# Optimization experiments

Hardware: AMD Instinct MI355X
Metric: run time of the kernel (lower is better)

## Reference

```python
import jax, jax.numpy as jnp
import numpy as np

N = 4096   # patients
D = 256    # encoding dim per modality
EPS = 1e-8 # torch CosineSimilarity eps


def setup_inputs() -> dict:
    key = jax.random.key(0)
    ks = jax.random.split(key, 7)
    return {
        "log_hazard": jax.random.normal(ks[0], (N,), dtype=jnp.float32),
        "time": jax.random.randint(ks[1], (N,), 0, 3650, dtype=jnp.int32),
        "event": jax.random.randint(ks[2], (N,), 0, 2, dtype=jnp.int32),
        "eb0": jax.random.normal(ks[3], (N, D), dtype=jnp.float32),
        "eb1": jax.random.normal(ks[4], (N, D), dtype=jnp.float32),
        "eb2": jax.random.normal(ks[5], (N, D), dtype=jnp.float32),
        "eb3": jax.random.normal(ks[6], (N, D), dtype=jnp.float32),
        "M_margin": 1,
    }


def _cox_npll(h, t, e):
    # risk_matrix = (outer(t,t) >= t^2).T  ->  risk[i,j] = (t_j * t_i >= t_i^2)
    tt = t[:, None] * t[None, :]                      # [N,N] = t_i * t_j
    risk = (tt >= (t * t)[:, None]).astype(h.dtype)   # row i: patients j with t_j >= t_i
    log_denom = jnp.log(risk @ jnp.exp(h))            # [N]
    ef = e.astype(h.dtype)
    return -jnp.sum(ef * (h - log_denom)) / jnp.sum(ef)


def _similarity_loss(blocks, margin):
    # Vectorized form of the O(N^2 * n_mod) pairwise loop.
    matched = jnp.zeros((N, N), dtype=blocks[0].dtype)  # sum_mod cos(x_i, x_j) over valid mods
    own = jnp.zeros((N, N), dtype=blocks[0].dtype)      # sum_mod cos(x_i, x_i) over valid mods
    for x in blocks:
        nrm = jnp.linalg.norm(x, axis=1)                # [N]
        den = jnp.maximum(nrm, EPS)
        xn = x / den[:, None]
        S = xn @ xn.T                                   # cos(x_i, x_j) with torch eps semantics
        diag = (nrm * nrm) / (den * den)                # cos(x_i, x_i)
        miss = jnp.all(x == x[:, :1], axis=1)           # modality missing (constant row)
        valid = (~(miss[:, None] | miss[None, :])).astype(x.dtype)
        matched = matched + valid * S
        own = own + valid * diag[:, None]
    offdiag = 1.0 - jnp.eye(N, dtype=matched.dtype)
    per_pair = jax.nn.relu(margin - matched + own)
    return jnp.sum(offdiag * per_pair)


def reference(log_hazard, time, event, eb0, eb1, eb2, eb3, M_margin):
    margin = jnp.float32(M_margin)
    cox = _cox_npll(log_hazard, time, event)
    sim = _similarity_loss([eb0, eb1, eb2, eb3], margin)
    return cox + sim
```

## Files before the change

kernel.cpp:

```cpp
#include <hip/hip_runtime.h>
#include <stdint.h>

#define NPAT 4096
#define DIM  256
#define KB   1024
#define EPSV 1e-8f
#define BT   64
#define BKB  128
#define NT   (NPAT / BT)
#define NBLK (NT * (NT + 1) / 2)
#define NBINS 4096

typedef float f32x4 __attribute__((ext_vector_type(4)));

#define WS_DVAL_OFF 256
#define WS_MVEC_OFF (WS_DVAL_OFF + 16*NPAT)
#define WS_XN_OFF   (WS_MVEC_OFF + 16*NPAT)

__device__ __forceinline__ void gl_lds16(const uint8_t* g, uint8_t* l) {
  __builtin_amdgcn_global_load_lds(
      (const __attribute__((address_space(1))) void*)g,
      (__attribute__((address_space(3))) void*)l, 16, 0, 0);
}

__device__ __forceinline__ float decode_margin(const int* pm) {
  int v = *pm;
  if (v > -16777216 && v < 16777216) return (float)v;
  return __int_as_float(v);
}

__global__ __launch_bounds__(256) void prep_kernel(
    const float4* __restrict__ eb0, const float4* __restrict__ eb1,
    const float4* __restrict__ eb2, const float4* __restrict__ eb3,
    uint8_t* __restrict__ Xn, float* __restrict__ dval_f,
    float* __restrict__ mvec_f, float* __restrict__ scal)
{
  const int i    = blockIdx.x;
  const int wv   = threadIdx.x >> 6;
  const int lane = threadIdx.x & 63;
  const float4* ebs[4] = {eb0, eb1, eb2, eb3};
  const float4 v = ebs[wv][i * (DIM / 4) + lane];
  float s = v.x * v.x + v.y * v.y + v.z * v.z + v.w * v.w;
#pragma unroll
  for (int o = 32; o; o >>= 1) s += __shfl_down(s, o, 64);
  s = __shfl(s, 0, 64);
  const float x0 = __shfl(v.x, 0, 64);
  const bool eq = (v.x == x0) && (v.y == x0) && (v.z == x0) && (v.w == x0);
  const bool miss = (__ballot(eq) == ~0ull);
  const float nrm = sqrtf(s);
  const float den = fmaxf(nrm, EPSV);
  const float inv = miss ? 0.0f : (1.0f / den);
  int p = 0;
  p = __builtin_amdgcn_cvt_pk_fp8_f32(v.x * inv, v.y * inv, p, false);
  p = __builtin_amdgcn_cvt_pk_fp8_f32(v.z * inv, v.w * inv, p, true);
  *(int*)&Xn[(size_t)i * KB + wv * DIM + lane * 4] = p;
  if (lane == 0) {
    const float diag = (nrm * nrm) / (den * den);
    dval_f[i * 4 + wv] = miss ? 0.0f : diag;
    mvec_f[i * 4 + wv] = miss ? 0.0f : 1.0f;
  }
  if (i == 0 && threadIdx.x == 0) scal[0] = 0.0f;
}

__global__ __launch_bounds__(256, 8) void sim_gemm_kernel(
    const uint8_t* __restrict__ Xn, const float4* __restrict__ dval,
    const float4* __restrict__ mvec, const int* __restrict__ pmargin,
    float* __restrict__ sim_acc)
{
  __shared__ __align__(16) uint8_t lA[BT * BKB];
  __shared__ __align__(16) uint8_t lB[BT * BKB];
  __shared__ float wred[4];

  const int L = blockIdx.x;
  int bi = (int)((2 * NT + 1 - sqrtf((float)((2 * NT + 1) * (2 * NT + 1)) - 8.0f * L)) * 0.5f);
  if (bi < 0) bi = 0;
  if (bi > NT - 1) bi = NT - 1;
  while (bi > 0 && bi * NT - bi * (bi - 1) / 2 > L) --bi;
  while ((bi + 1) * NT - (bi + 1) * bi / 2 <= L) ++bi;
  const int bj = bi + (L - (bi * NT - bi * (bi - 1) / 2));

  const int tid = threadIdx.x;
  const int lane = tid & 63, wvv = tid >> 6;
  const int wi = wvv >> 1, wj = wvv & 1;

  const int r0 = tid >> 3;
  const int p16 = ((tid & 7) ^ (r0 & 7)) * 16;
  const uint8_t* gA = Xn + (size_t)(bi * BT) * KB;
  const uint8_t* gB = Xn + (size_t)(bj * BT) * KB;

  f32x4 acc[2][2] = {};
  const int mrow = lane & 15, kg = lane >> 4;
  const int rA0 = wi * 32 + mrow;
  const int rB0 = wj * 32 + mrow;
  const int swA7 = (rA0 & 7), swB7 = (rB0 & 7);

  for (int k0 = 0; k0 < KB; k0 += BKB) {
    __syncthreads();
    gl_lds16(gA + (size_t)r0 * KB        + k0 + p16, &lA[tid * 16]);
    gl_lds16(gA + (size_t)(r0 + 32) * KB + k0 + p16, &lA[4096 + tid * 16]);
    gl_lds16(gB + (size_t)r0 * KB        + k0 + p16, &lB[tid * 16]);
    gl_lds16(gB + (size_t)(r0 + 32) * KB + k0 + p16, &lB[4096 + tid * 16]);
    __syncthreads();
#pragma unroll
    for (int t = 0; t < 4; ++t) {
      const int c = t * 4 + kg;
      const int half = (c & 1) * 8, sw = c >> 1;
      const int oA = ((sw ^ swA7) * 16) + half;
      const int oB = ((sw ^ swB7) * 16) + half;
      const long a0 = *(const long*)&lA[rA0 * BKB + oA];
      const long a1 = *(const long*)&lA[(rA0 + 16) * BKB + oA];
      const long b0 = *(const long*)&lB[rB0 * BKB + oB];
      const long b1 = *(const long*)&lB[(rB0 + 16) * BKB + oB];
      acc[0][0] = __builtin_amdgcn_mfma_f32_16x16x32_fp8_fp8(a0, b0, acc[0][0], 0, 0, 0);
      acc[0][1] = __builtin_amdgcn_mfma_f32_16x16x32_fp8_fp8(a0, b1, acc[0][1], 0, 0, 0);
      acc[1][0] = __builtin_amdgcn_mfma_f32_16x16x32_fp8_fp8(a1, b0, acc[1][0], 0, 0, 0);
      acc[1][1] = __builtin_amdgcn_mfma_f32_16x16x32_fp8_fp8(a1, b1, acc[1][1], 0, 0, 0);
    }
  }

  __syncthreads();
  float4* eRDi = (float4*)lA;
  float4* eCMi = (float4*)lA + 64;
  float4* eRDj = (float4*)lA + 128;
  float4* eCMj = (float4*)lA + 192;
  if (tid < 64) {
    eRDi[tid] = dval[bi * BT + tid];
    eCMi[tid] = mvec[bi * BT + tid];
  } else if (tid < 128) {
    const int s = tid - 64;
    eRDj[s] = dval[bj * BT + s];
    eCMj[s] = mvec[bj * BT + s];
  }
  __syncthreads();

  const float margin = decode_margin(pmargin);
  const bool isDiag = (bi == bj);
  float local = 0.0f;
  const int rq = (lane >> 4) * 4;
  const int cc = lane & 15;
#pragma unroll
  for (int mi = 0; mi < 2; ++mi) {
#pragma unroll
    for (int mj = 0; mj < 2; ++mj) {
      const int jl = wj * 32 + mj * 16 + cc;
      const float4 cmj = eCMj[jl];
      const float4 rdj = eRDj[jl];
#pragma unroll
      for (int r = 0; r < 4; ++r) {
        const int il = wi * 32 + mi * 16 + rq + r;
        const float4 rdi = eRDi[il];
        const float sv = acc[mi][mj][r];
        const float own_ij = rdi.x * cmj.x + rdi.y * cmj.y + rdi.z * cmj.z + rdi.w * cmj.w;
        const float v1 = fmaxf(margin - sv + own_ij, 0.0f);
        local += (isDiag && il == jl) ? 0.0f : v1;
        if (!isDiag) {
          const float4 cmi = eCMi[il];
          const float own_ji = rdj.x * cmi.x + rdj.y * cmi.y + rdj.z * cmi.z + rdj.w * cmi.w;
          local += fmaxf(margin - sv + own_ji, 0.0f);
        }
      }
    }
  }
#pragma unroll
  for (int o = 32; o; o >>= 1) local += __shfl_down(local, o, 64);
  if (lane == 0) wred[wvv] = local;
  __syncthreads();
  if (tid == 0) atomicAdd(sim_acc, wred[0] + wred[1] + wred[2] + wred[3]);
}

__global__ __launch_bounds__(1024) void cox_kernel(
    const float* __restrict__ h, const int* __restrict__ t,
    const int* __restrict__ e, const float* __restrict__ scal,
    float* __restrict__ out)
{
  __shared__ float bins[NBINS];
  __shared__ float p[1024];
  __shared__ float rn[16], rd[16];
  const int tid = threadIdx.x;
#pragma unroll
  for (int k = 0; k < 4; ++k) bins[tid + k * 1024] = 0.0f;
  __syncthreads();
#pragma unroll
  for (int k = 0; k < 4; ++k) {
    const int i = tid + k * 1024;
    atomicAdd(&bins[t[i]], expf(h[i]));
  }
  __syncthreads();
  const float b0 = bins[4 * tid], b1 = bins[4 * tid + 1];
  const float b2 = bins[4 * tid + 2], b3 = bins[4 * tid + 3];
  const float part = b0 + b1 + b2 + b3;
  p[tid] = part;
  __syncthreads();
  for (int off = 1; off < 1024; off <<= 1) {
    const float v = p[tid];
    const float a = (tid + off < 1024) ? p[tid + off] : 0.0f;
    __syncthreads();
    p[tid] = v + a;
    __syncthreads();
  }
  const float above = p[tid] - part;
  const float s3 = above + b3, s2 = s3 + b2, s1 = s2 + b1, s0 = s1 + b0;
  bins[4 * tid] = s0; bins[4 * tid + 1] = s1;
  bins[4 * tid + 2] = s2; bins[4 * tid + 3] = s3;
  __syncthreads();
  float nloc = 0.0f, dloc = 0.0f;
#pragma unroll
  for (int k = 0; k < 4; ++k) {
    const int i = tid + k * 1024;
    const float ei = (float)e[i];
    if (ei != 0.0f) { nloc += ei * (h[i] - logf(bins[t[i]])); dloc += ei; }
  }
  const int lane = tid & 63, w = tid >> 6;
#pragma unroll
  for (int o = 32; o; o >>= 1) {
    nloc += __shfl_down(nloc, o, 64);
    dloc += __shfl_down(dloc, o, 64);
  }
  if (lane == 0) { rn[w] = nloc; rd[w] = dloc; }
  __syncthreads();
  if (tid == 0) {
    float n = 0.0f, d = 0.0f;
#pragma unroll
    for (int k = 0; k < 16; ++k) { n += rn[k]; d += rd[k]; }
    out[0] = scal[0] - n / d;
  }
}

extern "C" void kernel_launch(void* const* d_in, const int* in_sizes, int n_in,
                              void* d_out, int out_size, void* d_ws, size_t ws_size,
                              hipStream_t stream) {
  const float* h    = (const float*)d_in[0];
  const int*   t    = (const int*)  d_in[1];
  const int*   e    = (const int*)  d_in[2];
  const float4* eb0 = (const float4*)d_in[3];
  const float4* eb1 = (const float4*)d_in[4];
  const float4* eb2 = (const float4*)d_in[5];
  const float4* eb3 = (const float4*)d_in[6];
  const int*   pm   = (const int*)  d_in[7];

  char*    ws   = (char*)d_ws;
  float*   scal = (float*)ws;
  float*   dvf  = (float*)(ws + WS_DVAL_OFF);
  float*   mvf  = (float*)(ws + WS_MVEC_OFF);
  uint8_t* Xn   = (uint8_t*)(ws + WS_XN_OFF);

  prep_kernel<<<NPAT, 256, 0, stream>>>(eb0, eb1, eb2, eb3, Xn, dvf, mvf, scal);
  sim_gemm_kernel<<<NBLK, 256, 0, stream>>>(Xn, (const float4*)dvf, (const float4*)mvf, pm, &scal[0]);
  cox_kernel<<<1, 1024, 0, stream>>>(h, t, e, scal, (float*)d_out);
}
```

Baseline: 133.6 us.

## Enlarge GEMM tile to 128, load fragments directly from global, reorder cox kernel

The similarity GEMM tile grows from 64 to 128 rows. The LDS staging with global_load_lds is replaced by direct per-lane 16-byte global loads into MFMA fragments, and each wave now holds a 4x4 accumulator grid. The change cuts the block count and the per-k-step barriers and raises arithmetic intensity per block, at the cost of more registers, lower occupancy and uncoalesced row-strided global reads that rely on L2. The cox kernel now runs before the GEMM and writes its term to workspace, and a tiny finalize kernel combines the two terms, adding one launch.

```diff
diff --git a/kernel.cpp b/kernel.cpp
--- a/kernel.cpp
+++ b/kernel.cpp
@@ -5,23 +5,17 @@
 #define DIM  256
 #define KB   1024
 #define EPSV 1e-8f
-#define BT   64
-#define BKB  128
+#define BT   128
 #define NT   (NPAT / BT)
 #define NBLK (NT * (NT + 1) / 2)
 #define NBINS 4096
 
 typedef float f32x4 __attribute__((ext_vector_type(4)));
+typedef long  lng2  __attribute__((ext_vector_type(2)));
 
 #define WS_DVAL_OFF 256
 #define WS_MVEC_OFF (WS_DVAL_OFF + 16*NPAT)
 #define WS_XN_OFF   (WS_MVEC_OFF + 16*NPAT)
-
-__device__ __forceinline__ void gl_lds16(const uint8_t* g, uint8_t* l) {
-  __builtin_amdgcn_global_load_lds(
-      (const __attribute__((address_space(1))) void*)g,
-      (__attribute__((address_space(3))) void*)l, 16, 0, 0);
-}
 
 __device__ __forceinline__ float decode_margin(const int* pm) {
   int v = *pm;
@@ -62,14 +56,13 @@
   if (i == 0 && threadIdx.x == 0) scal[0] = 0.0f;
 }
 
-__global__ __launch_bounds__(256, 8) void sim_gemm_kernel(
+__global__ __launch_bounds__(256, 4) void sim_gemm_kernel(
     const uint8_t* __restrict__ Xn, const float4* __restrict__ dval,
     const float4* __restrict__ mvec, const int* __restrict__ pmargin,
     float* __restrict__ sim_acc)
 {
-  __shared__ __align__(16) uint8_t lA[BT * BKB];
-  __shared__ __align__(16) uint8_t lB[BT * BKB];
-  __shared__ float wred[4];
+  __shared__ float4 eRDi[BT], eCMi[BT], eRDj[BT], eCMj[BT];
+  __shared__ float  wred[4];
 
   const int L = blockIdx.x;
   int bi = (int)((2 * NT + 1 - sqrtf((float)((2 * NT + 1) * (2 * NT + 1)) - 8.0f * L)) * 0.5f);
@@ -82,52 +75,41 @@
   const int tid = threadIdx.x;
   const int lane = tid & 63, wvv = tid >> 6;
   const int wi = wvv >> 1, wj = wvv & 1;
-
-  const int r0 = tid >> 3;
-  const int p16 = ((tid & 7) ^ (r0 & 7)) * 16;
-  const uint8_t* gA = Xn + (size_t)(bi * BT) * KB;
-  const uint8_t* gB = Xn + (size_t)(bj * BT) * KB;
-
-  f32x4 acc[2][2] = {};
   const int mrow = lane & 15, kg = lane >> 4;
-  const int rA0 = wi * 32 + mrow;
-  const int rB0 = wj * 32 + mrow;
-  const int swA7 = (rA0 & 7), swB7 = (rB0 & 7);
-
-  for (int k0 = 0; k0 < KB; k0 += BKB) {
-    __syncthreads();
-    gl_lds16(gA + (size_t)r0 * KB        + k0 + p16, &lA[tid * 16]);
-    gl_lds16(gA + (size_t)(r0 + 32) * KB + k0 + p16, &lA[4096 + tid * 16]);
-    gl_lds16(gB + (size_t)r0 * KB        + k0 + p16, &lB[tid * 16]);
-    gl_lds16(gB + (size_t)(r0 + 32) * KB + k0 + p16, &lB[4096 + tid * 16]);
-    __syncthreads();
-#pragma unroll
-    for (int t = 0; t < 4; ++t) {
-      const int c = t * 4 + kg;
-      const int half = (c & 1) * 8, sw = c >> 1;
-      const int oA = ((sw ^ swA7) * 16) + half;
-      const int oB = ((sw ^ swB7) * 16) + half;
-      const long a0 = *(const long*)&lA[rA0 * BKB + oA];
-      const long a1 = *(const long*)&lA[(rA0 + 16) * BKB + oA];
-      const long b0 = *(const long*)&lB[rB0 * BKB + oB];
-      const long b1 = *(const long*)&lB[(rB0 + 16) * BKB + oB];
-      acc[0][0] = __builtin_amdgcn_mfma_f32_16x16x32_fp8_fp8(a0, b0, acc[0][0], 0, 0, 0);
-      acc[0][1] = __builtin_amdgcn_mfma_f32_16x16x32_fp8_fp8(a0, b1, acc[0][1], 0, 0, 0);
-      acc[1][0] = __builtin_amdgcn_mfma_f32_16x16x32_fp8_fp8(a1, b0, acc[1][0], 0, 0, 0);
-      acc[1][1] = __builtin_amdgcn_mfma_f32_16x16x32_fp8_fp8(a1, b1, acc[1][1], 0, 0, 0);
-    }
-  }
-
-  __syncthreads();
-  float4* eRDi = (float4*)lA;
-  float4* eCMi = (float4*)lA + 64;
-  float4* eRDj = (float4*)lA + 128;
-  float4* eCMj = (float4*)lA + 192;
-  if (tid < 64) {
+
+  const uint8_t* pA[4];
+  const uint8_t* pB[4];
+#pragma unroll
+  for (int mi = 0; mi < 4; ++mi)
+    pA[mi] = Xn + (size_t)(bi * BT + wi * 64 + mi * 16 + mrow) * KB + kg * 16;
+#pragma unroll
+  for (int mj = 0; mj < 4; ++mj)
+    pB[mj] = Xn + (size_t)(bj * BT + wj * 64 + mj * 16 + mrow) * KB + kg * 16;
+
+  f32x4 acc[4][4] = {};
+
+#pragma unroll
+  for (int ks = 0; ks < 16; ++ks) {
+    lng2 af[4], bf[4];
+#pragma unroll
+    for (int mi = 0; mi < 4; ++mi) af[mi] = *(const lng2*)(pA[mi] + ks * 64);
+#pragma unroll
+    for (int mj = 0; mj < 4; ++mj) bf[mj] = *(const lng2*)(pB[mj] + ks * 64);
+#pragma unroll
+    for (int h = 0; h < 2; ++h)
+#pragma unroll
+      for (int mi = 0; mi < 4; ++mi)
+#pragma unroll
+        for (int mj = 0; mj < 4; ++mj)
+          acc[mi][mj] = __builtin_amdgcn_mfma_f32_16x16x32_fp8_fp8(
+              af[mi][h], bf[mj][h], acc[mi][mj], 0, 0, 0);
+  }
+
+  if (tid < BT) {
     eRDi[tid] = dval[bi * BT + tid];
     eCMi[tid] = mvec[bi * BT + tid];
-  } else if (tid < 128) {
-    const int s = tid - 64;
+  } else {
+    const int s = tid - BT;
     eRDj[s] = dval[bj * BT + s];
     eCMj[s] = mvec[bj * BT + s];
   }
@@ -139,15 +121,15 @@
   const int rq = (lane >> 4) * 4;
   const int cc = lane & 15;
 #pragma unroll
-  for (int mi = 0; mi < 2; ++mi) {
-#pragma unroll
-    for (int mj = 0; mj < 2; ++mj) {
-      const int jl = wj * 32 + mj * 16 + cc;
+  for (int mi = 0; mi < 4; ++mi) {
+#pragma unroll
+    for (int mj = 0; mj < 4; ++mj) {
+      const int jl = wj * 64 + mj * 16 + cc;
       const float4 cmj = eCMj[jl];
       const float4 rdj = eRDj[jl];
 #pragma unroll
       for (int r = 0; r < 4; ++r) {
-        const int il = wi * 32 + mi * 16 + rq + r;
+        const int il = wi * 64 + mi * 16 + rq + r;
         const float4 rdi = eRDi[il];
         const float sv = acc[mi][mj][r];
         const float own_ij = rdi.x * cmj.x + rdi.y * cmj.y + rdi.z * cmj.z + rdi.w * cmj.w;
@@ -170,8 +152,7 @@
 
 __global__ __launch_bounds__(1024) void cox_kernel(
     const float* __restrict__ h, const int* __restrict__ t,
-    const int* __restrict__ e, const float* __restrict__ scal,
-    float* __restrict__ out)
+    const int* __restrict__ e, float* __restrict__ scal)
 {
   __shared__ float bins[NBINS];
   __shared__ float p[1024];
@@ -222,8 +203,12 @@
     float n = 0.0f, d = 0.0f;
 #pragma unroll
     for (int k = 0; k < 16; ++k) { n += rn[k]; d += rd[k]; }
-    out[0] = scal[0] - n / d;
-  }
+    scal[1] = n / d;
+  }
+}
+
+__global__ void finalize_kernel(const float* __restrict__ scal, float* __restrict__ out) {
+  out[0] = scal[0] - scal[1];
 }
 
 extern "C" void kernel_launch(void* const* d_in, const int* in_sizes, int n_in,
@@ -245,6 +230,7 @@
   uint8_t* Xn   = (uint8_t*)(ws + WS_XN_OFF);
 
   prep_kernel<<<NPAT, 256, 0, stream>>>(eb0, eb1, eb2, eb3, Xn, dvf, mvf, scal);
+  cox_kernel<<<1, 1024, 0, stream>>>(h, t, e, scal);
   sim_gemm_kernel<<<NBLK, 256, 0, stream>>>(Xn, (const float4*)dvf, (const float4*)mvf, pm, &scal[0]);
-  cox_kernel<<<1, 1024, 0, stream>>>(h, t, e, scal, (float*)d_out);
-}
+  finalize_kernel<<<1, 1, 0, stream>>>(scal, (float*)d_out);
+}
```

Measured after the change: 140.3 us. 1.05x slower.
